# Kernel tuning notes

Hardware: AMD Instinct MI355X
Metric: run time of the kernel (lower is better)

The kernel has to match this reference:

```python
import jax, jax.numpy as jnp
import numpy as np

D_MODEL = 1024
N_HEADS = 16
HEAD_DIM = D_MODEL // N_HEADS
B, T = 2, 2048


def _rotate_half(x):
    # Faithful to module's _apply_rotary: view (..., D//2, 2), pair -> (-x1, x0)
    xr = x.reshape(*x.shape[:-1], HEAD_DIM // 2, 2)
    rot = jnp.stack([-xr[..., 1], xr[..., 0]], axis=-1)
    return rot.reshape(*x.shape)


def setup_inputs() -> dict:
    key = jax.random.key(0)
    ks = jax.random.split(key, 9)
    s = 1.0 / np.sqrt(D_MODEL)
    return {
        "x": jax.random.normal(ks[0], (B, T, D_MODEL), jnp.float32),
        "Wq": jax.random.normal(ks[1], (D_MODEL, D_MODEL), jnp.float32) * s,
        "bq": jax.random.normal(ks[2], (D_MODEL,), jnp.float32) * 0.02,
        "Wk": jax.random.normal(ks[3], (D_MODEL, D_MODEL), jnp.float32) * s,
        "bk": jax.random.normal(ks[4], (D_MODEL,), jnp.float32) * 0.02,
        "Wv": jax.random.normal(ks[5], (D_MODEL, D_MODEL), jnp.float32) * s,
        "bv": jax.random.normal(ks[6], (D_MODEL,), jnp.float32) * 0.02,
        "Wo": jax.random.normal(ks[7], (D_MODEL, D_MODEL), jnp.float32) * s,
        "bo": jax.random.normal(ks[8], (D_MODEL,), jnp.float32) * 0.02,
    }


def reference(x, Wq, bq, Wk, bk, Wv, bv, Wo, bo):
    b, t, _ = x.shape
    # QKV projections (nn.Linear: x @ W.T + b), split heads -> (B, H, T, Dh)
    def proj(W, bias):
        y = x @ W.T + bias
        return y.reshape(b, t, N_HEADS, HEAD_DIM).transpose(0, 2, 1, 3)

    q = _rotate_half(proj(Wq, bq))
    k = _rotate_half(proj(Wk, bk))
    v = proj(Wv, bv)

    scale = 1.0 / jnp.sqrt(jnp.asarray(HEAD_DIM, x.dtype))
    scores = jnp.einsum('bhqd,bhkd->bhqk', q, k) * scale
    causal = jnp.tril(jnp.ones((t, t), bool))  # (T, T)
    scores = jnp.where(causal, scores, jnp.asarray(-jnp.inf, scores.dtype))
    attn = jax.nn.softmax(scores, axis=-1)
    out = jnp.einsum('bhqk,bhkd->bhqd', attn, v)
    out = out.transpose(0, 2, 1, 3).reshape(b, t, D_MODEL)
    return out @ Wo.T + bo
```

## Files before the change

kernel.cpp:

```cpp
#include <hip/hip_runtime.h>
#include <stdint.h>

#define DM 1024
#define NH 16
#define HD 64
#define BB 2
#define TT 2048
#define MT (BB*TT)

typedef __bf16 bfrag __attribute__((ext_vector_type(8)));
typedef float  f32x4 __attribute__((ext_vector_type(4)));

__device__ __forceinline__ unsigned short f2bf(float f) {
  union { float f; unsigned u; } v; v.f = f;
  unsigned r = v.u + 0x7fffu + ((v.u >> 16) & 1u);
  return (unsigned short)(r >> 16);
}

__device__ __forceinline__ unsigned short f2bf_hw(float f) {
  __bf16 b = (__bf16)f;
  union { __bf16 b; unsigned short u; } v; v.b = b;
  return v.u;
}

__device__ __forceinline__ unsigned int pack2bf(float a, float b) {
  union { __bf16 h[2]; unsigned int u; } v;
  v.h[0] = (__bf16)a; v.h[1] = (__bf16)b;
  return v.u;
}

__device__ __forceinline__ void async16(const void* g, void* l) {
  __builtin_amdgcn_global_load_lds(
      (const __attribute__((address_space(1))) unsigned int*)g,
      (__attribute__((address_space(3))) unsigned int*)l, 16, 0, 0);
}

#define CBAR() do { asm volatile("" ::: "memory"); \
                    __builtin_amdgcn_s_barrier();  \
                    asm volatile("" ::: "memory"); } while (0)

#define QSCALE 0.18033688011112043f
#define M2BIAS 15.869645449778597f

__global__ __launch_bounds__(256) void cvt_kernel(
    const float* __restrict__ x,  const float* __restrict__ Wq,
    const float* __restrict__ Wk, const float* __restrict__ Wv,
    const float* __restrict__ Wo,
    unsigned short* __restrict__ xb, unsigned short* __restrict__ wqkv,
    unsigned short* __restrict__ wob) {
  int i = blockIdx.x * 256 + threadIdx.x;
  const int NX = MT * DM / 4;
  const int NW = DM * DM / 4;
  const float* src; unsigned short* dst; int off;
  if      (i < NX)        { src = x;  dst = xb;              off = i; }
  else if (i < NX + NW)   { src = Wq; dst = wqkv;            off = i - NX; }
  else if (i < NX + 2*NW) { src = Wk; dst = wqkv + DM*DM;    off = i - NX - NW; }
  else if (i < NX + 3*NW) { src = Wv; dst = wqkv + 2*DM*DM;  off = i - NX - 2*NW; }
  else                    { src = Wo; dst = wob;             off = i - NX - 3*NW; }
  float4 v = ((const float4*)src)[off];
  ushort4 o;
  o.x = f2bf(v.x); o.y = f2bf(v.y); o.z = f2bf(v.z); o.w = f2bf(v.w);
  ((ushort4*)dst)[off] = o;
}

__global__ __launch_bounds__(512, 2) void gemm_qkv(
    const unsigned short* __restrict__ A, const unsigned short* __restrict__ Bm,
    const float* __restrict__ bias0, const float* __restrict__ bias1,
    const float* __restrict__ bias2,
    unsigned short* __restrict__ Qo, unsigned short* __restrict__ Ko,
    unsigned short* __restrict__ Vo) {
  const int tid = threadIdx.x;
  const int wave = tid >> 6, lane = tid & 63;
  const int lr = lane & 15, quad = lane >> 4;
  const int flat = blockIdx.x;
  const int s = (flat & 7) * 32 + (flat >> 3);
  const int m0 = (s & 15) * 256, n0 = (s >> 4) * 192;

  __shared__ __align__(16) unsigned short sA[2][2][256 * 32];
  __shared__ __align__(16) unsigned short sB[2][2][192 * 32];

  const f32x4 zero = {0.f, 0.f, 0.f, 0.f};
  f32x4 acc[4][6];
#pragma unroll
  for (int i = 0; i < 4; i++)
#pragma unroll
    for (int j = 0; j < 6; j++) acc[i][j] = zero;

  const int wm = (wave >> 1) * 64, wn = (wave & 1) * 96;

  auto stagePart = [&](int h) {
    if (h >= 64) return;
    const int ts = h >> 2, pi = h & 3;
    const int buf = ts & 1, hk = pi >> 1;
    const int k0 = ts * 64 + (hk << 5);
    if (pi & 1) {
      unsigned short* dst = &sB[buf][hk][0];
      {
        int fb = wave * 512;
        int fl = fb + lane * 8;
        int row = fl >> 5, c = (fl >> 3) & 3;
        async16(Bm + (size_t)(n0 + row) * 1024 + k0 + ((c ^ ((row >> 1) & 3)) << 3),
                dst + fb);
      }
      if (wave < 4) {
        int fb = 4096 + wave * 512;
        int fl = fb + lane * 8;
        int row = fl >> 5, c = (fl >> 3) & 3;
        async16(Bm + (size_t)(n0 + row) * 1024 + k0 + ((c ^ ((row >> 1) & 3)) << 3),
                dst + fb);
      }
    } else {
      unsigned short* dst = &sA[buf][hk][0];
#pragma unroll
      for (int rep = 0; rep < 2; ++rep) {
        int fb = rep * 4096 + wave * 512;
        int fl = fb + lane * 8;
        int row = fl >> 5, c = (fl >> 3) & 3;
        async16(A + (size_t)(m0 + row) * 1024 + k0 + ((c ^ ((row >> 1) & 3)) << 3),
                dst + fb);
      }
    }
  };

#pragma unroll
  for (int h = 0; h < 6; ++h) stagePart(h);
  asm volatile("s_waitcnt vmcnt(6)" ::: "memory");
  CBAR();

  bfrag af[4], bf[3];
#pragma unroll 1
  for (int t = 0; t < 16; ++t) {
    const int buf = t & 1;
    const int P0 = 4 * t;

    auto rdA = [&](int hk) {
#pragma unroll
      for (int i = 0; i < 4; i++) {
        int ra = wm + i * 16 + lr;
        af[i] = *(const bfrag*)&sA[buf][hk][ra * 32 + ((quad ^ ((ra >> 1) & 3)) << 3)];
      }
    };
    auto rdB = [&](int hk, int jh) {
#pragma unroll
      for (int jj = 0; jj < 3; jj++) {
        int rb = wn + (jh * 3 + jj) * 16 + lr;
        bf[jj] = *(const bfrag*)&sB[buf][hk][rb * 32 + ((quad ^ ((rb >> 1) & 3)) << 3)];
      }
    };
    auto domfma = [&](int jh) {
      __builtin_amdgcn_s_setprio(1);
#pragma unroll
      for (int i = 0; i < 4; i++)
#pragma unroll
        for (int jj = 0; jj < 3; jj++)
          acc[i][jh * 3 + jj] = __builtin_amdgcn_mfma_f32_16x16x32_bf16(
              af[i], bf[jj], acc[i][jh * 3 + jj], 0, 0, 0);
      __builtin_amdgcn_s_setprio(0);
    };

    rdA(0); rdB(0, 0);
    stagePart(P0 + 6);
    CBAR();
    domfma(0);
    rdB(0, 1);
    stagePart(P0 + 7);
    if (t == 15) { asm volatile("s_waitcnt vmcnt(0)" ::: "memory"); }
    else         { asm volatile("s_waitcnt vmcnt(6)" ::: "memory"); }
    CBAR();
    domfma(1);
    rdA(1); rdB(1, 0);
    stagePart(P0 + 8);
    CBAR();
    domfma(0);
    rdB(1, 1);
    stagePart(P0 + 9);
    if (t == 14)      { asm volatile("s_waitcnt vmcnt(3)" ::: "memory"); }
    else if (t < 14)  { asm volatile("s_waitcnt vmcnt(6)" ::: "memory"); }
    CBAR();
    domfma(1);
  }

#pragma unroll
  for (int j = 0; j < 6; j++) {
    int n = n0 + wn + j * 16 + lr;
    int qkv = n >> 10, nn = n & 1023;
    float bias = (qkv == 0 ? bias0 : qkv == 1 ? bias1 : bias2)[nn];
    int h = nn >> 6, d = nn & 63;
    if (qkv == 2) {
#pragma unroll
      for (int i = 0; i < 4; i++) {
        int t0 = m0 + wm + i * 16 + quad * 4;
        int b = t0 >> 11, tt = t0 & 2047;
        size_t bb = (size_t)((b << 4) + h) * (TT * 64);
        int kk0 = tt & 63;
        size_t off = bb + (size_t)(tt >> 6) * 4096 +
                     (size_t)((kk0 >> 3) << 9) + (d << 3) + (kk0 & 7);
        ushort4 pk;
        pk.x = f2bf(acc[i][j][0] + bias);
        pk.y = f2bf(acc[i][j][1] + bias);
        pk.z = f2bf(acc[i][j][2] + bias);
        pk.w = f2bf(acc[i][j][3] + bias);
        *(ushort4*)(Vo + off) = pk;
      }
    } else {
#pragma unroll
      for (int i = 0; i < 4; i++)
#pragma unroll
        for (int r = 0; r < 4; r++) {
          int m = m0 + wm + i * 16 + quad * 4 + r;
          float vb = acc[i][j][r] + bias;
          float pv = __shfl_xor(vb, 1);
          float val = (n & 1) ? pv : -pv;
          int b = m >> 11, t = m & 2047;
          size_t base = (size_t)((b << 4) + h) * (TT * 64);
          if (qkv == 0) {
            Qo[base + (size_t)t * 64 + d] = f2bf(val * QSCALE);
          } else {
            int kk = t & 63;
            size_t off = base + (size_t)(t >> 6) * 4096 +
                         (size_t)((d >> 3) << 9) + (kk << 3) + (d & 7);
            Ko[off] = f2bf(val);
          }
        }
    }
  }
}

__global__ __launch_bounds__(256) void gemm_op(
    const unsigned short* __restrict__ A, const unsigned short* __restrict__ Bm,
    const float* __restrict__ bias0, float* __restrict__ Co) {
  const int tid = threadIdx.x;
  const int wave = tid >> 6, lane = tid & 63;
  const int lr = lane & 15, quad = lane >> 4;
  const int m0 = blockIdx.y * 64, n0 = blockIdx.x * 128;
  __shared__ __align__(16) unsigned short sA[2][64 * 64];
  __shared__ __align__(16) unsigned short sB[2][128 * 64];
  const f32x4 zero = {0.f, 0.f, 0.f, 0.f};
  f32x4 acc[2][4];
#pragma unroll
  for (int i = 0; i < 2; i++)
#pragma unroll
    for (int j = 0; j < 4; j++) acc[i][j] = zero;
  const int wm = (wave >> 1) * 32, wn = (wave & 1) * 64;

  auto swz = [](int row) { return ((row & 1) << 2) | ((row >> 1) & 3); };

  auto stage = [&](int kt, int buf) {
    const int k0 = kt * 64;
#pragma unroll
    for (int rep = 0; rep < 2; ++rep) {
      int fb = rep * 2048 + wave * 512;
      int fl = fb + lane * 8;
      int row = fl >> 6, pc = (fl >> 3) & 7;
      async16(A + (size_t)(m0 + row) * 1024 + k0 + ((pc ^ swz(row)) << 3), &sA[buf][fb]);
    }
#pragma unroll
    for (int rep = 0; rep < 4; ++rep) {
      int fb = rep * 2048 + wave * 512;
      int fl = fb + lane * 8;
      int row = fl >> 6, pc = (fl >> 3) & 7;
      async16(Bm + (size_t)(n0 + row) * 1024 + k0 + ((pc ^ swz(row)) << 3), &sB[buf][fb]);
    }
  };

  stage(0, 0);
  for (int kt = 0; kt < 16; ++kt) {
    const int buf = kt & 1;
    __syncthreads();
    if (kt + 1 < 16) stage(kt + 1, buf ^ 1);
#pragma unroll
    for (int ks = 0; ks < 2; ++ks) {
      bfrag af[2], bfr[4];
#pragma unroll
      for (int i = 0; i < 2; i++) {
        int ra = wm + i * 16 + lr;
        af[i] = *(const bfrag*)&sA[buf][ra * 64 + (((ks * 4 + quad) ^ swz(ra)) << 3)];
      }
#pragma unroll
      for (int j = 0; j < 4; j++) {
        int rb = wn + j * 16 + lr;
        bfr[j] = *(const bfrag*)&sB[buf][rb * 64 + (((ks * 4 + quad) ^ swz(rb)) << 3)];
      }
#pragma unroll
      for (int i = 0; i < 2; i++)
#pragma unroll
        for (int j = 0; j < 4; j++)
          acc[i][j] = __builtin_amdgcn_mfma_f32_16x16x32_bf16(af[i], bfr[j], acc[i][j], 0, 0, 0);
    }
  }

#pragma unroll
  for (int j = 0; j < 4; j++) {
    int n = n0 + wn + j * 16 + lr;
    float bias = bias0[n];
#pragma unroll
    for (int i = 0; i < 2; i++)
#pragma unroll
      for (int r = 0; r < 4; r++) {
        int m = m0 + wm + i * 16 + quad * 4 + r;
        Co[(size_t)m * 1024 + n] = acc[i][j][r] + bias;
      }
  }
}

__global__ __launch_bounds__(256, 4) void flash_kernel(
    const unsigned short* __restrict__ Qg, const unsigned short* __restrict__ Kg,
    const unsigned short* __restrict__ Vg, unsigned short* __restrict__ Og) {
  const int flat = blockIdx.x;
  const int xcd = flat & 7;
  const int seq = flat >> 3;
  const int bh = (seq >> 5) * 8 + xcd;
  const int qt = 31 - (seq & 31);
  const int tid = threadIdx.x, wave = tid >> 6, lane = tid & 63;
  const int lr = lane & 15, quad = lane >> 4;
  __shared__ __align__(16) unsigned short sK[2][4096];
  __shared__ __align__(16) unsigned short sV[2][4096];
  __shared__ __align__(16) unsigned short sP[4][1024];
  const size_t base = (size_t)bh * (TT * 64);
  const int nS = qt + 1;
  const int qg = qt * 64 + wave * 16 + lr;
  const f32x4 zero = {0.f, 0.f, 0.f, 0.f};

  bfrag qf0, qf1;
  {
    const unsigned short* qr = Qg + base + (size_t)qg * 64;
    qf0 = *(const bfrag*)(qr + quad * 8);
    qf1 = *(const bfrag*)(qr + 32 + quad * 8);
  }
  f32x4 o[4];
  float rs = 0.f;
#pragma unroll
  for (int j = 0; j < 4; j++) o[j] = zero;

  const unsigned short* kgb = Kg + base;
  const unsigned short* vgb = Vg + base;

#pragma unroll
  for (int rep = 0; rep < 2; ++rep) {
    int fb = rep * 2048 + wave * 512;
    async16(kgb + fb + lane * 8, &sK[0][fb]);
    async16(vgb + fb + lane * 8, &sV[0][fb]);
  }

  const int pwr = lr * 8 + (quad & 1) * 4;
  const int pq2 = quad >> 1;

  for (int kt = 0; kt < nS; ++kt) {
    const int buf = kt & 1;
    __syncthreads();
    if (kt + 1 < nS) {
#pragma unroll
      for (int rep = 0; rep < 2; ++rep) {
        int fb = rep * 2048 + wave * 512;
        const size_t g = (size_t)(kt + 1) * 4096 + fb + lane * 8;
        async16(kgb + g, &sK[buf ^ 1][fb]);
        async16(vgb + g, &sV[buf ^ 1][fb]);
      }
    }
    f32x4 sT[4];
    __builtin_amdgcn_s_setprio(1);
#pragma unroll
    for (int ct = 0; ct < 4; ct++) {
      int row8 = (ct * 16 + lr) * 8;
      bfrag k0 = *(const bfrag*)&sK[buf][quad * 512 + row8];
      bfrag k1 = *(const bfrag*)&sK[buf][(4 + quad) * 512 + row8];
      f32x4 t = __builtin_amdgcn_mfma_f32_16x16x32_bf16(k0, qf0, zero, 0, 0, 0);
      sT[ct]  = __builtin_amdgcn_mfma_f32_16x16x32_bf16(k1, qf1, t,    0, 0, 0);
    }
    __builtin_amdgcn_s_setprio(0);
    const bool diag = (kt == qt);
#pragma unroll
    for (int ct = 0; ct < 4; ++ct) {
      float e[4];
#pragma unroll
      for (int r = 0; r < 4; ++r)
        e[r] = exp2f(sT[ct][r] - M2BIAS);
      if (diag) {
#pragma unroll
        for (int r = 0; r < 4; ++r) {
          int key = kt * 64 + ct * 16 + quad * 4 + r;
          if (key > qg) e[r] = 0.f;
        }
      }
      rs += (e[0] + e[1]) + (e[2] + e[3]);
      uint2 w;
      w.x = pack2bf(e[0], e[1]);
      w.y = pack2bf(e[2], e[3]);
      *(uint2*)&sP[wave][(ct * 2 + pq2) * 128 + pwr] = w;
    }
    bfrag pf0 = *(const bfrag*)&sP[wave][quad * 128 + lr * 8];
    bfrag pf1 = *(const bfrag*)&sP[wave][(4 + quad) * 128 + lr * 8];
    __builtin_amdgcn_s_setprio(1);
#pragma unroll
    for (int j = 0; j < 4; j++) {
      int row8 = (j * 16 + lr) * 8;
      bfrag v0 = *(const bfrag*)&sV[buf][quad * 512 + row8];
      bfrag v1 = *(const bfrag*)&sV[buf][(4 + quad) * 512 + row8];
      o[j] = __builtin_amdgcn_mfma_f32_16x16x32_bf16(v0, pf0, o[j], 0, 0, 0);
      o[j] = __builtin_amdgcn_mfma_f32_16x16x32_bf16(v1, pf1, o[j], 0, 0, 0);
    }
    __builtin_amdgcn_s_setprio(0);
  }

  rs += __shfl_xor(rs, 16); rs += __shfl_xor(rs, 32);
  const float inv = 1.0f / rs;

  const int b = bh >> 4, h = bh & 15;
#pragma unroll
  for (int j = 0; j < 4; j++) {
    ushort4 pk;
    pk.x = f2bf_hw(o[j][0] * inv); pk.y = f2bf_hw(o[j][1] * inv);
    pk.z = f2bf_hw(o[j][2] * inv); pk.w = f2bf_hw(o[j][3] * inv);
    int col = h * 64 + j * 16 + quad * 4;
    *(ushort4*)(Og + (size_t)(b * TT + qg) * 1024 + col) = pk;
  }
}

extern "C" void kernel_launch(void* const* d_in, const int* in_sizes, int n_in,
                              void* d_out, int out_size, void* d_ws, size_t ws_size,
                              hipStream_t stream) {
  const float* x  = (const float*)d_in[0];
  const float* Wq = (const float*)d_in[1];
  const float* bq = (const float*)d_in[2];
  const float* Wk = (const float*)d_in[3];
  const float* bk = (const float*)d_in[4];
  const float* Wv = (const float*)d_in[5];
  const float* bv = (const float*)d_in[6];
  const float* Wo = (const float*)d_in[7];
  const float* bo = (const float*)d_in[8];
  float* out = (float*)d_out;

  unsigned short* ws = (unsigned short*)d_ws;
  unsigned short* xb   = ws;
  unsigned short* wqkv = ws + (size_t)4 * 1024 * 1024;
  unsigned short* wob  = ws + (size_t)7 * 1024 * 1024;
  unsigned short* Qb   = ws + (size_t)8 * 1024 * 1024;
  unsigned short* Kb   = ws + (size_t)12 * 1024 * 1024;
  unsigned short* Vb   = ws + (size_t)16 * 1024 * 1024;
  unsigned short* Ob   = ws + (size_t)20 * 1024 * 1024;

  cvt_kernel<<<dim3(8192), dim3(256), 0, stream>>>(x, Wq, Wk, Wv, Wo, xb, wqkv, wob);
  gemm_qkv<<<dim3(256), dim3(512), 0, stream>>>(xb, wqkv, bq, bk, bv, Qb, Kb, Vb);
  flash_kernel<<<dim3(1024), dim3(256), 0, stream>>>(Qb, Kb, Vb, Ob);
  gemm_op<<<dim3(8, 64), dim3(256), 0, stream>>>(Ob, wob, bo, out);
}
```

Measured before the change: 210.7 us.

## Load K/V fragments directly from global into registers, drop LDS double buffer

The flash attention kernel no longer stages K and V tiles through double-buffered shared memory with async copies and per-tile barriers. Each wave now loads its K/V MFMA fragments straight from global memory, relying on the cache, since all four waves read the same tile. The intent is to remove the __syncthreads and LDS traffic and free shared memory. The query-tile ordering also alternates between ascending and descending across head groups to balance causal work. The risk is redundant global and cache traffic and exposed load latency, because there is no explicit prefetch and the loop is forced to unroll 1.

New measurement: 187.1 us. 1.13x faster.

```diff
diff --git a/kernel.cpp b/kernel.cpp
--- a/kernel.cpp
+++ b/kernel.cpp
@@ -308,13 +308,13 @@
     const unsigned short* __restrict__ Vg, unsigned short* __restrict__ Og) {
   const int flat = blockIdx.x;
   const int xcd = flat & 7;
-  const int seq = flat >> 3;
-  const int bh = (seq >> 5) * 8 + xcd;
-  const int qt = 31 - (seq & 31);
+  const int idx = flat >> 3;
+  const int g   = idx >> 5;
+  const int bh  = g * 8 + xcd;
+  const int a   = idx & 31;
+  const int qt  = (g & 1) ? (31 - a) : a;
   const int tid = threadIdx.x, wave = tid >> 6, lane = tid & 63;
   const int lr = lane & 15, quad = lane >> 4;
-  __shared__ __align__(16) unsigned short sK[2][4096];
-  __shared__ __align__(16) unsigned short sV[2][4096];
   __shared__ __align__(16) unsigned short sP[4][1024];
   const size_t base = (size_t)bh * (TT * 64);
   const int nS = qt + 1;
@@ -334,38 +334,32 @@
 
   const unsigned short* kgb = Kg + base;
   const unsigned short* vgb = Vg + base;
-
-#pragma unroll
-  for (int rep = 0; rep < 2; ++rep) {
-    int fb = rep * 2048 + wave * 512;
-    async16(kgb + fb + lane * 8, &sK[0][fb]);
-    async16(vgb + fb + lane * 8, &sV[0][fb]);
-  }
+  const int lko = quad * 512 + lr * 8;
 
   const int pwr = lr * 8 + (quad & 1) * 4;
   const int pq2 = quad >> 1;
 
+#pragma unroll 1
   for (int kt = 0; kt < nS; ++kt) {
-    const int buf = kt & 1;
-    __syncthreads();
-    if (kt + 1 < nS) {
-#pragma unroll
-      for (int rep = 0; rep < 2; ++rep) {
-        int fb = rep * 2048 + wave * 512;
-        const size_t g = (size_t)(kt + 1) * 4096 + fb + lane * 8;
-        async16(kgb + g, &sK[buf ^ 1][fb]);
-        async16(vgb + g, &sV[buf ^ 1][fb]);
-      }
+    const unsigned short* kt_k = kgb + (size_t)kt * 4096;
+    const unsigned short* kt_v = vgb + (size_t)kt * 4096;
+    bfrag kf0[4], kf1[4], vf0[4], vf1[4];
+#pragma unroll
+    for (int ct = 0; ct < 4; ct++) {
+      kf0[ct] = *(const bfrag*)(kt_k + lko + ct * 128);
+      kf1[ct] = *(const bfrag*)(kt_k + 2048 + lko + ct * 128);
+    }
+#pragma unroll
+    for (int j = 0; j < 4; j++) {
+      vf0[j] = *(const bfrag*)(kt_v + lko + j * 128);
+      vf1[j] = *(const bfrag*)(kt_v + 2048 + lko + j * 128);
     }
     f32x4 sT[4];
     __builtin_amdgcn_s_setprio(1);
 #pragma unroll
     for (int ct = 0; ct < 4; ct++) {
-      int row8 = (ct * 16 + lr) * 8;
-      bfrag k0 = *(const bfrag*)&sK[buf][quad * 512 + row8];
-      bfrag k1 = *(const bfrag*)&sK[buf][(4 + quad) * 512 + row8];
-      f32x4 t = __builtin_amdgcn_mfma_f32_16x16x32_bf16(k0, qf0, zero, 0, 0, 0);
-      sT[ct]  = __builtin_amdgcn_mfma_f32_16x16x32_bf16(k1, qf1, t,    0, 0, 0);
+      f32x4 t = __builtin_amdgcn_mfma_f32_16x16x32_bf16(kf0[ct], qf0, zero, 0, 0, 0);
+      sT[ct]  = __builtin_amdgcn_mfma_f32_16x16x32_bf16(kf1[ct], qf1, t,    0, 0, 0);
     }
     __builtin_amdgcn_s_setprio(0);
     const bool diag = (kt == qt);
@@ -393,11 +387,8 @@
     __builtin_amdgcn_s_setprio(1);
 #pragma unroll
     for (int j = 0; j < 4; j++) {
-      int row8 = (j * 16 + lr) * 8;
-      bfrag v0 = *(const bfrag*)&sV[buf][quad * 512 + row8];
-      bfrag v1 = *(const bfrag*)&sV[buf][(4 + quad) * 512 + row8];
-      o[j] = __builtin_amdgcn_mfma_f32_16x16x32_bf16(v0, pf0, o[j], 0, 0, 0);
-      o[j] = __builtin_amdgcn_mfma_f32_16x16x32_bf16(v1, pf1, o[j], 0, 0, 0);
+      o[j] = __builtin_amdgcn_mfma_f32_16x16x32_bf16(vf0[j], pf0, o[j], 0, 0, 0);
+      o[j] = __builtin_amdgcn_mfma_f32_16x16x32_bf16(vf1[j], pf1, o[j], 0, 0, 0);
     }
     __builtin_amdgcn_s_setprio(0);
   }
```
